# Optimization experiments

Hardware: AMD Instinct MI355X
Metric: run time of the kernel (lower is better)

Reference implementation:

```python
import jax, jax.numpy as jnp
import numpy as np

H = 64  # hidden size


def _gru_cell(x, h, Wih, Whh, bih, bhh):
    """PyTorch-convention GRU cell. x:[B,in], h:[B,H]. Gate order: r, z, n."""
    gi = x @ Wih.T + bih              # [B, 3H]
    gh = h @ Whh.T + bhh              # [B, 3H]
    ir, iz, in_ = jnp.split(gi, 3, axis=-1)
    hr, hz, hn = jnp.split(gh, 3, axis=-1)
    r = jax.nn.sigmoid(ir + hr)
    z = jax.nn.sigmoid(iz + hz)
    n = jnp.tanh(in_ + r * hn)
    return (1.0 - z) * n + z * h


def setup_inputs() -> dict:
    key = jax.random.key(0)
    B, T, NIN = 4096, 256, 6
    ks = jax.random.split(key, 24)

    def w(k, shape, fan):
        return (jax.random.normal(k, shape, jnp.float32) / np.sqrt(fan).astype(np.float32))

    inp = {"x": jax.random.normal(ks[0], (B, T, NIN), jnp.float32)}
    # encoder layer 0 (input 6) and layer 1 (input 64)
    inp["enc_Wih0"] = w(ks[1], (3 * H, NIN), H)
    inp["enc_Whh0"] = w(ks[2], (3 * H, H), H)
    inp["enc_bih0"] = w(ks[3], (3 * H,), H)
    inp["enc_bhh0"] = w(ks[4], (3 * H,), H)
    inp["enc_Wih1"] = w(ks[5], (3 * H, H), H)
    inp["enc_Whh1"] = w(ks[6], (3 * H, H), H)
    inp["enc_bih1"] = w(ks[7], (3 * H,), H)
    inp["enc_bhh1"] = w(ks[8], (3 * H,), H)
    # decoder layer 0 (input 1) and layer 1 (input 64)
    inp["dec_Wih0"] = w(ks[9], (3 * H, 1), H)
    inp["dec_Whh0"] = w(ks[10], (3 * H, H), H)
    inp["dec_bih0"] = w(ks[11], (3 * H,), H)
    inp["dec_bhh0"] = w(ks[12], (3 * H,), H)
    inp["dec_Wih1"] = w(ks[13], (3 * H, H), H)
    inp["dec_Whh1"] = w(ks[14], (3 * H, H), H)
    inp["dec_bih1"] = w(ks[15], (3 * H,), H)
    inp["dec_bhh1"] = w(ks[16], (3 * H,), H)
    # output head
    inp["out_W"] = w(ks[17], (1, H), H)
    inp["out_b"] = w(ks[18], (1,), H)
    inp["target_len"] = 180
    return inp


def reference(x, enc_Wih0, enc_Whh0, enc_bih0, enc_bhh0,
              enc_Wih1, enc_Whh1, enc_bih1, enc_bhh1,
              dec_Wih0, dec_Whh0, dec_bih0, dec_bhh0,
              dec_Wih1, dec_Whh1, dec_bih1, dec_bhh1,
              out_W, out_b, target_len):
    B = x.shape[0]
    dtype = x.dtype

    # ---- encoder: 2-layer GRU over x, return final hidden per layer ----
    seq = jnp.swapaxes(x, 0, 1)  # [T, B, 6] time-major
    enc_layers = [(enc_Wih0, enc_Whh0, enc_bih0, enc_bhh0),
                  (enc_Wih1, enc_Whh1, enc_bih1, enc_bhh1)]
    h_finals = []
    for (Wih, Whh, bih, bhh) in enc_layers:
        def step(h, xt, Wih=Wih, Whh=Whh, bih=bih, bhh=bhh):
            hn = _gru_cell(xt, h, Wih, Whh, bih, bhh)
            return hn, hn
        h_last, seq = jax.lax.scan(step, jnp.zeros((B, H), dtype), seq)
        h_finals.append(h_last)

    def dec_step(carry, _):
        h0, h1, prev = carry
        h0 = _gru_cell(prev, h0, dec_Wih0, dec_Whh0, dec_bih0, dec_bhh0)
        h1 = _gru_cell(h0, h1, dec_Wih1, dec_Whh1, dec_bih1, dec_bhh1)
        cv = h1 @ out_W.T + out_b  # [B, 1]
        return (h0, h1, cv), cv

    prev0 = jnp.zeros((B, 1), dtype)
    _, outs = jax.lax.scan(dec_step, (h_finals[0], h_finals[1], prev0),
                           None, length=target_len)
    return jnp.swapaxes(outs, 0, 1)  # [B, target_len, 1]
```

## Files before the change

kernel.cpp:

```cpp
#include <hip/hip_runtime.h>
#include <cstdint>

typedef _Float16 half8 __attribute__((ext_vector_type(8)));
typedef __attribute__((ext_vector_type(4))) float floatx4;
typedef unsigned int uint;

#define TSEQ 256
#define TDEC 180
#define NIN  6
#define GROWS 16
#define NBLK (4096 / GROWS)
#define RS0 104
#define RS1 72

__device__ __forceinline__ floatx4 mfma16(half8 a, half8 b, floatx4 c) {
  return __builtin_amdgcn_mfma_f32_16x16x32_f16(a, b, c, 0, 0, 0);
}

__device__ __forceinline__ float sigm(float v) {
  return __builtin_amdgcn_rcpf(1.0f + __builtin_amdgcn_exp2f(-1.4426950408889634f * v));
}
__device__ __forceinline__ float tanh_fast(float v) {
  return 2.0f * __builtin_amdgcn_rcpf(1.0f + __builtin_amdgcn_exp2f(-2.8853900817779268f * v)) - 1.0f;
}

__device__ __forceinline__ half8 ldh8(const _Float16* p) { return *(const half8*)p; }

#define PASS2(F0, F1, r, z, g, W) do {                                  \
  r = mfma16(F0, W[0][0], r); z = mfma16(F0, W[1][0], z); g = mfma16(F0, W[2][0], g); \
  r = mfma16(F1, W[0][1], r); z = mfma16(F1, W[1][1], z); g = mfma16(F1, W[2][1], g); \
} while (0)

#define PASS1(F0, r, z, g, W) do {                                      \
  r = mfma16(F0, W[0][0], r); z = mfma16(F0, W[1][0], z); g = mfma16(F0, W[2][0], g); \
} while (0)

__device__ __forceinline__ void pollge1(const volatile uint* p, uint need4) {
  for (;;) {
    if (*p >= need4) break;
    __builtin_amdgcn_s_sleep(1);
  }
  asm volatile("" ::: "memory");
}

__global__ void __launch_bounds__(512, 2)
gru_persist(const float* __restrict__ x,
            const float* __restrict__ eWih0, const float* __restrict__ eWhh0,
            const float* __restrict__ ebih0, const float* __restrict__ ebhh0,
            const float* __restrict__ eWih1, const float* __restrict__ eWhh1,
            const float* __restrict__ ebih1, const float* __restrict__ ebhh1,
            const float* __restrict__ dWih0, const float* __restrict__ dWhh0,
            const float* __restrict__ dbih0, const float* __restrict__ dbhh0,
            const float* __restrict__ dWih1, const float* __restrict__ dWhh1,
            const float* __restrict__ dbih1, const float* __restrict__ dbhh1,
            const float* __restrict__ outW, const float* __restrict__ outB,
            float* __restrict__ out)
{
  __shared__ __align__(16) _Float16 s0[2][16][RS0];
  __shared__ __align__(16) _Float16 s1[2][16][RS1];
  __shared__ __align__(16) uint prog[16];

  const int tid  = threadIdx.x;
  const bool isA = tid < 256;
  const int wvL  = (tid >> 6) & 3;
  const int lane = tid & 63;
  const int c    = lane & 15;
  const int q    = lane >> 4;
  const int u    = wvL * 16 + c;
  const long base = (long)blockIdx.x * GROWS;

  const volatile uint* asum = (const volatile uint*)&prog[0];
  const volatile uint* bsum = (const volatile uint*)&prog[8];
  uint* mysum = (uint*)&prog[isA ? 0 : 8];

  for (int i = tid; i < 2 * 16 * RS0; i += 512) ((uint16_t*)s0)[i] = 0;
  for (int i = tid; i < 2 * 16 * RS1; i += 512) ((uint16_t*)s1)[i] = 0;
  if (tid < 16) prog[tid] = 0;
  if (tid < GROWS * NIN) {
    int m = tid / 6, i2 = tid - m * 6;
    s0[0][m][64 + i2] = (_Float16)x[(base + m) * (TSEQ * NIN) + i2];
  }

  half8 W1[3][2];
  half8 W2[3][2];
  float hr[4] = {0, 0, 0, 0};

  auto loadW64 = [&](const float* W, half8 (&D)[3][2]) {
    #pragma unroll
    for (int s = 0; s < 3; s++) {
      const int n = (s * 4 + wvL) * 16 + c;
      #pragma unroll
      for (int kt = 0; kt < 2; kt++) {
        const int k0 = kt * 32 + q * 8;
        #pragma unroll
        for (int j = 0; j < 8; j++) D[s][kt][j] = (_Float16)W[n * 64 + k0 + j];
      }
    }
  };

  float cR, cZ, c3, c4;
  if (isA) {
    loadW64(eWhh0, W1);
    #pragma unroll
    for (int s = 0; s < 3; s++) {
      const int n = (s * 4 + wvL) * 16 + c;
      #pragma unroll
      for (int kt = 0; kt < 2; kt++)
        #pragma unroll
        for (int j = 0; j < 8; j++) {
          float v = (kt == 0 && q == 0 && j < NIN) ? eWih0[n * NIN + j] : 0.0f;
          W2[s][kt][j] = (_Float16)v;
        }
    }
    cR = ebih0[u] + ebhh0[u];
    cZ = ebih0[64 + u] + ebhh0[64 + u];
    c3 = ebhh0[128 + u];
    c4 = ebih0[128 + u];
  } else {
    loadW64(eWih1, W1); loadW64(eWhh1, W2);
    cR = ebih1[u] + ebhh1[u];
    cZ = ebih1[64 + u] + ebhh1[64 + u];
    c3 = ebih1[128 + u];
    c4 = ebhh1[128 + u];
  }
  __syncthreads();

  if (isA) {
    const bool doX = (wvL == 0) && (lane < 48);
    const float *px0 = nullptr, *px1 = nullptr;
    int xo0 = 0, xo1 = 0; float xn0 = 0.f, xn1 = 0.f;
    if (doX) {
      int s0_ = lane, s1_ = lane + 48;
      int m0 = s0_ / 6, i0 = s0_ - m0 * 6, m1 = s1_ / 6, i1 = s1_ - m1 * 6;
      px0 = x + (base + m0) * (TSEQ * NIN) + i0;
      px1 = x + (base + m1) * (TSEQ * NIN) + i1;
      xo0 = m0 * RS0 + 64 + i0; xo1 = m1 * RS0 + 64 + i1;
      xn0 = px0[NIN]; xn1 = px1[NIN];
    }
    for (int i = 0; i < TSEQ; i += 2) {
      #pragma unroll
      for (int h2 = 0; h2 < 2; h2++) {
        const int i_ = i + h2, p = h2, pn = h2 ^ 1;
        pollge1(asum, 4u * (uint)i_);
        const half8 a0 = ldh8(&s0[p][c][q * 8]);
        const half8 a1 = ldh8(&s0[p][c][32 + q * 8]);
        const half8 xf = ldh8(&s0[p][c][64 + q * 8]);
        floatx4 aR = {cR, cR, cR, cR}, aZ = {cZ, cZ, cZ, cZ};
        floatx4 a3 = {c3, c3, c3, c3}, a4 = {c4, c4, c4, c4};
        PASS2(a0, a1, aR, aZ, a3, W1);
        PASS1(xf, aR, aZ, a4, W2);
        pollge1(bsum, 4u * (uint)(i_ > 0 ? i_ - 1 : 0));
        if (doX && i_ + 1 < TSEQ) {
          ((_Float16*)s0[pn])[xo0] = (_Float16)xn0;
          ((_Float16*)s0[pn])[xo1] = (_Float16)xn1;
          if (i_ + 2 < TSEQ) { xn0 = px0[(i_ + 2) * NIN]; xn1 = px1[(i_ + 2) * NIN]; }
        }
        #pragma unroll
        for (int r4 = 0; r4 < 4; r4++) {
          const float gr = sigm(aR[r4]);
          const float gz = sigm(aZ[r4]);
          const float nn = tanh_fast(a4[r4] + gr * a3[r4]);
          const float hn = nn + gz * (hr[r4] - nn);
          hr[r4] = hn;
          s0[pn][q * 4 + r4][u] = (_Float16)hn;
        }
        asm volatile("s_waitcnt lgkmcnt(0)" ::: "memory");
        if (lane == 0) atomicAdd(mysum, 1u);
      }
    }
    loadW64(dWhh0, W1);
    const float ob = outB[0];
    #pragma unroll
    for (int s = 0; s < 3; s++) {
      const int n = (s * 4 + wvL) * 16 + c;
      const float wd = dWih0[n];
      #pragma unroll
      for (int kt = 0; kt < 2; kt++) {
        const int k0 = kt * 32 + q * 8;
        #pragma unroll
        for (int j = 0; j < 8; j++) W2[s][kt][j] = (_Float16)(wd * outW[k0 + j]);
      }
    }
    const float bR0 = dbih0[u] + dbhh0[u];
    const float bZ0 = dbih0[64 + u] + dbhh0[64 + u];
    const float b30 = dbhh0[128 + u];
    const float b40 = dbih0[128 + u];
    cR = bR0 + dWih0[u] * ob;
    cZ = bZ0 + dWih0[64 + u] * ob;
    c3 = b30;
    c4 = b40 + dWih0[128 + u] * ob;
    for (int i = TSEQ; i < TSEQ + TDEC; i += 2) {
      #pragma unroll
      for (int h2 = 0; h2 < 2; h2++) {
        const int i_ = i + h2, p = h2, pn = h2 ^ 1;
        const bool first = (i_ == TSEQ);
        pollge1(asum, 4u * (uint)i_);
        const half8 a0 = ldh8(&s0[p][c][q * 8]);
        const half8 a1 = ldh8(&s0[p][c][32 + q * 8]);
        const float vR = first ? bR0 : cR, vZ = first ? bZ0 : cZ, v4 = first ? b40 : c4;
        floatx4 aR = {vR, vR, vR, vR}, aZ = {vZ, vZ, vZ, vZ};
        floatx4 a3 = {c3, c3, c3, c3}, a4 = {v4, v4, v4, v4};
        PASS2(a0, a1, aR, aZ, a3, W1);
        pollge1(bsum, 4u * (uint)(first ? i_ - 1 : i_));
        if (!first) {
          const half8 b0 = ldh8(&s1[p][c][q * 8]);
          const half8 b1 = ldh8(&s1[p][c][32 + q * 8]);
          PASS2(b0, b1, aR, aZ, a4, W2);
        }
        #pragma unroll
        for (int r4 = 0; r4 < 4; r4++) {
          const float gr = sigm(aR[r4]);
          const float gz = sigm(aZ[r4]);
          const float nn = tanh_fast(a4[r4] + gr * a3[r4]);
          const float hn = nn + gz * (hr[r4] - nn);
          hr[r4] = hn;
          s0[pn][q * 4 + r4][u] = (_Float16)hn;
        }
        asm volatile("s_waitcnt lgkmcnt(0)" ::: "memory");
        if (lane == 0) atomicAdd(mysum, 1u);
      }
    }
  } else {
    const float ob = outB[0];
    float wk[2][8];
    #pragma unroll
    for (int kt = 0; kt < 2; kt++)
      #pragma unroll
      for (int j = 0; j < 8; j++) wk[kt][j] = outW[kt * 32 + q * 8 + j];

    for (int i = 0; i < TSEQ; i += 2) {
      #pragma unroll
      for (int h2 = 0; h2 < 2; h2++) {
        const int i_ = i + h2, p = h2, pn = h2 ^ 1;
        pollge1(bsum, 4u * (uint)i_);
        const half8 f0 = ldh8(&s1[p][c][q * 8]);
        const half8 f1 = ldh8(&s1[p][c][32 + q * 8]);
        floatx4 aR = {cR, cR, cR, cR}, aZ = {cZ, cZ, cZ, cZ};
        floatx4 a3 = {c3, c3, c3, c3}, a4 = {c4, c4, c4, c4};
        PASS2(f0, f1, aR, aZ, a4, W2);
        pollge1(asum, 4u * (uint)(i_ + 1));
        const half8 g0 = ldh8(&s0[pn][c][q * 8]);
        const half8 g1 = ldh8(&s0[pn][c][32 + q * 8]);
        PASS2(g0, g1, aR, aZ, a3, W1);
        #pragma unroll
        for (int r4 = 0; r4 < 4; r4++) {
          const float gr = sigm(aR[r4]);
          const float gz = sigm(aZ[r4]);
          const float nn = tanh_fast(a3[r4] + gr * a4[r4]);
          const float hn = nn + gz * (hr[r4] - nn);
          hr[r4] = hn;
          s1[pn][q * 4 + r4][u] = (_Float16)hn;
        }
        asm volatile("s_waitcnt lgkmcnt(0)" ::: "memory");
        if (lane == 0) atomicAdd(mysum, 1u);
      }
    }
    loadW64(dWih1, W1); loadW64(dWhh1, W2);
    cR = dbih1[u] + dbhh1[u];
    cZ = dbih1[64 + u] + dbhh1[64 + u];
    c3 = dbih1[128 + u]; c4 = dbhh1[128 + u];
    for (int i = TSEQ; i < TSEQ + TDEC; i += 2) {
      #pragma unroll
      for (int h2 = 0; h2 < 2; h2++) {
        const int i_ = i + h2, p = h2, pn = h2 ^ 1;
        pollge1(bsum, 4u * (uint)i_);
        const half8 f0 = ldh8(&s1[p][c][q * 8]);
        const half8 f1 = ldh8(&s1[p][c][32 + q * 8]);
        floatx4 aR = {cR, cR, cR, cR}, aZ = {cZ, cZ, cZ, cZ};
        floatx4 a3 = {c3, c3, c3, c3}, a4 = {c4, c4, c4, c4};
        PASS2(f0, f1, aR, aZ, a4, W2);
        if (wvL == 0 && i_ > TSEQ) {
          float cv = 0.0f;
          #pragma unroll
          for (int j = 0; j < 8; j++) {
            cv = fmaf((float)f0[j], wk[0][j], cv);
            cv = fmaf((float)f1[j], wk[1][j], cv);
          }
          cv += __shfl_xor(cv, 16);
          cv += __shfl_xor(cv, 32);
          if (lane < 16) out[(base + lane) * TDEC + (i_ - TSEQ - 1)] = cv + ob;
        }
        pollge1(asum, 4u * (uint)(i_ + 1));
        const half8 g0 = ldh8(&s0[pn][c][q * 8]);
        const half8 g1 = ldh8(&s0[pn][c][32 + q * 8]);
        PASS2(g0, g1, aR, aZ, a3, W1);
        #pragma unroll
        for (int r4 = 0; r4 < 4; r4++) {
          const float gr = sigm(aR[r4]);
          const float gz = sigm(aZ[r4]);
          const float nn = tanh_fast(a3[r4] + gr * a4[r4]);
          const float hn = nn + gz * (hr[r4] - nn);
          hr[r4] = hn;
          s1[pn][q * 4 + r4][u] = (_Float16)hn;
        }
        asm volatile("s_waitcnt lgkmcnt(0)" ::: "memory");
        if (lane == 0) atomicAdd(mysum, 1u);
      }
    }
    if (wvL == 0) {
      pollge1(bsum, 4u * (uint)(TSEQ + TDEC));
      const half8 f0 = ldh8(&s1[0][c][q * 8]);
      const half8 f1 = ldh8(&s1[0][c][32 + q * 8]);
      float cv = 0.0f;
      #pragma unroll
      for (int j = 0; j < 8; j++) {
        cv = fmaf((float)f0[j], wk[0][j], cv);
        cv = fmaf((float)f1[j], wk[1][j], cv);
      }
      cv += __shfl_xor(cv, 16);
      cv += __shfl_xor(cv, 32);
      if (lane < 16) out[(base + lane) * TDEC + (TDEC - 1)] = cv + ob;
    }
  }
}

extern "C" void kernel_launch(void* const* d_in, const int* in_sizes, int n_in,
                              void* d_out, int out_size, void* d_ws, size_t ws_size,
                              hipStream_t stream) {
  (void)in_sizes; (void)n_in; (void)d_ws; (void)ws_size; (void)out_size;
  const float* x     = (const float*)d_in[0];
  const float* eWih0 = (const float*)d_in[1];
  const float* eWhh0 = (const float*)d_in[2];
  const float* ebih0 = (const float*)d_in[3];
  const float* ebhh0 = (const float*)d_in[4];
  const float* eWih1 = (const float*)d_in[5];
  const float* eWhh1 = (const float*)d_in[6];
  const float* ebih1 = (const float*)d_in[7];
  const float* ebhh1 = (const float*)d_in[8];
  const float* dWih0 = (const float*)d_in[9];
  const float* dWhh0 = (const float*)d_in[10];
  const float* dbih0 = (const float*)d_in[11];
  const float* dbhh0 = (const float*)d_in[12];
  const float* dWih1 = (const float*)d_in[13];
  const float* dWhh1 = (const float*)d_in[14];
  const float* dbih1 = (const float*)d_in[15];
  const float* dbhh1 = (const float*)d_in[16];
  const float* outW  = (const float*)d_in[17];
  const float* outB  = (const float*)d_in[18];
  hipLaunchKernelGGL(gru_persist, dim3(NBLK), dim3(512), 0, stream,
                     x, eWih0, eWhh0, ebih0, ebhh0, eWih1, eWhh1, ebih1, ebhh1,
                     dWih0, dWhh0, dbih0, dbhh0, dWih1, dWhh1, dbih1, dbhh1,
                     outW, outB, (float*)d_out);
}
```

Baseline: 411.0 us.

## Fold log2e scaling into weights, preload bias accumulators, peel first decoder steps

Pre-scales the gate weights and biases by log2(e) (twice that for the candidate gate) so sigmoid and tanh become exp2 calls with no per-element multiply. Bias vectors are kept as loop-invariant accumulator registers and fed as the MFMA C operand, which removes the per-step splat initialisation. The first two decoder steps of layer 0 are peeled so the steady-state loop has no 'first' branches. It also drops the explicit lgkmcnt(0) wait before the progress atomic and keeps only a compiler barrier, which risks a race if the LDS writes are not complete when the counter is published.

```diff
diff --git a/kernel.cpp b/kernel.cpp
--- a/kernel.cpp
+++ b/kernel.cpp
@@ -12,27 +12,33 @@
 #define NBLK (4096 / GROWS)
 #define RS0 104
 #define RS1 72
+#define L2E 1.4426950408889634f
 
 __device__ __forceinline__ floatx4 mfma16(half8 a, half8 b, floatx4 c) {
   return __builtin_amdgcn_mfma_f32_16x16x32_f16(a, b, c, 0, 0, 0);
 }
 
-__device__ __forceinline__ float sigm(float v) {
-  return __builtin_amdgcn_rcpf(1.0f + __builtin_amdgcn_exp2f(-1.4426950408889634f * v));
-}
-__device__ __forceinline__ float tanh_fast(float v) {
-  return 2.0f * __builtin_amdgcn_rcpf(1.0f + __builtin_amdgcn_exp2f(-2.8853900817779268f * v)) - 1.0f;
+__device__ __forceinline__ float sigm2(float v) {
+  return __builtin_amdgcn_rcpf(1.0f + __builtin_amdgcn_exp2f(-v));
+}
+__device__ __forceinline__ float tanh2(float v) {
+  return fmaf(2.0f, __builtin_amdgcn_rcpf(1.0f + __builtin_amdgcn_exp2f(-v)), -1.0f);
 }
 
 __device__ __forceinline__ half8 ldh8(const _Float16* p) { return *(const half8*)p; }
 
-#define PASS2(F0, F1, r, z, g, W) do {                                  \
-  r = mfma16(F0, W[0][0], r); z = mfma16(F0, W[1][0], z); g = mfma16(F0, W[2][0], g); \
-  r = mfma16(F1, W[0][1], r); z = mfma16(F1, W[1][1], z); g = mfma16(F1, W[2][1], g); \
+#define PASS2_I3(F0, F1, r, z, g, W, QR, QZ, QG) do {                   \
+  r = mfma16(F0, W[0][0], QR); z = mfma16(F0, W[1][0], QZ); g = mfma16(F0, W[2][0], QG); \
+  r = mfma16(F1, W[0][1], r);  z = mfma16(F1, W[1][1], z);  g = mfma16(F1, W[2][1], g);  \
 } while (0)
 
-#define PASS1(F0, r, z, g, W) do {                                      \
-  r = mfma16(F0, W[0][0], r); z = mfma16(F0, W[1][0], z); g = mfma16(F0, W[2][0], g); \
+#define PASS2_A2I1(F0, F1, r, z, g, W, QG) do {                         \
+  r = mfma16(F0, W[0][0], r); z = mfma16(F0, W[1][0], z); g = mfma16(F0, W[2][0], QG); \
+  r = mfma16(F1, W[0][1], r); z = mfma16(F1, W[1][1], z); g = mfma16(F1, W[2][1], g);  \
+} while (0)
+
+#define PASS1_A2I1(F0, r, z, g, W, QG) do {                             \
+  r = mfma16(F0, W[0][0], r); z = mfma16(F0, W[1][0], z); g = mfma16(F0, W[2][0], QG); \
 } while (0)
 
 __device__ __forceinline__ void pollge1(const volatile uint* p, uint need4) {
@@ -42,6 +48,8 @@
   }
   asm volatile("" ::: "memory");
 }
+
+#define PUBLISH() do { asm volatile("" ::: "memory"); if (lane == 0) atomicAdd(mysum, 1u); } while (0)
 
 __global__ void __launch_bounds__(512, 2)
 gru_persist(const float* __restrict__ x,
@@ -84,6 +92,7 @@
   half8 W1[3][2];
   half8 W2[3][2];
   float hr[4] = {0, 0, 0, 0};
+  const float SC[3] = {L2E, L2E, 2.0f * L2E};
 
   auto loadW64 = [&](const float* W, half8 (&D)[3][2]) {
     #pragma unroll
@@ -93,7 +102,7 @@
       for (int kt = 0; kt < 2; kt++) {
         const int k0 = kt * 32 + q * 8;
         #pragma unroll
-        for (int j = 0; j < 8; j++) D[s][kt][j] = (_Float16)W[n * 64 + k0 + j];
+        for (int j = 0; j < 8; j++) D[s][kt][j] = (_Float16)(SC[s] * W[n * 64 + k0 + j]);
       }
     }
   };
@@ -108,24 +117,26 @@
       for (int kt = 0; kt < 2; kt++)
         #pragma unroll
         for (int j = 0; j < 8; j++) {
-          float v = (kt == 0 && q == 0 && j < NIN) ? eWih0[n * NIN + j] : 0.0f;
+          float v = (kt == 0 && q == 0 && j < NIN) ? SC[s] * eWih0[n * NIN + j] : 0.0f;
           W2[s][kt][j] = (_Float16)v;
         }
     }
-    cR = ebih0[u] + ebhh0[u];
-    cZ = ebih0[64 + u] + ebhh0[64 + u];
-    c3 = ebhh0[128 + u];
-    c4 = ebih0[128 + u];
+    cR = L2E * (ebih0[u] + ebhh0[u]);
+    cZ = L2E * (ebih0[64 + u] + ebhh0[64 + u]);
+    c3 = 2.0f * L2E * ebhh0[128 + u];
+    c4 = 2.0f * L2E * ebih0[128 + u];
   } else {
     loadW64(eWih1, W1); loadW64(eWhh1, W2);
-    cR = ebih1[u] + ebhh1[u];
-    cZ = ebih1[64 + u] + ebhh1[64 + u];
-    c3 = ebih1[128 + u];
-    c4 = ebhh1[128 + u];
+    cR = L2E * (ebih1[u] + ebhh1[u]);
+    cZ = L2E * (ebih1[64 + u] + ebhh1[64 + u]);
+    c3 = 2.0f * L2E * ebih1[128 + u];
+    c4 = 2.0f * L2E * ebhh1[128 + u];
   }
   __syncthreads();
 
   if (isA) {
+    floatx4 QR = {cR, cR, cR, cR}, QZ = {cZ, cZ, cZ, cZ};
+    floatx4 Q3 = {c3, c3, c3, c3}, Q4 = {c4, c4, c4, c4};
     const bool doX = (wvL == 0) && (lane < 48);
     const float *px0 = nullptr, *px1 = nullptr;
     int xo0 = 0, xo1 = 0; float xn0 = 0.f, xn1 = 0.f;
@@ -145,10 +156,9 @@
         const half8 a0 = ldh8(&s0[p][c][q * 8]);
         const half8 a1 = ldh8(&s0[p][c][32 + q * 8]);
         const half8 xf = ldh8(&s0[p][c][64 + q * 8]);
-        floatx4 aR = {cR, cR, cR, cR}, aZ = {cZ, cZ, cZ, cZ};
-        floatx4 a3 = {c3, c3, c3, c3}, a4 = {c4, c4, c4, c4};
-        PASS2(a0, a1, aR, aZ, a3, W1);
-        PASS1(xf, aR, aZ, a4, W2);
+        floatx4 aR, aZ, a3, a4;
+        PASS2_I3(a0, a1, aR, aZ, a3, W1, QR, QZ, Q3);
+        PASS1_A2I1(xf, aR, aZ, a4, W2, Q4);
         pollge1(bsum, 4u * (uint)(i_ > 0 ? i_ - 1 : 0));
         if (doX && i_ + 1 < TSEQ) {
           ((_Float16*)s0[pn])[xo0] = (_Float16)xn0;
@@ -157,15 +167,14 @@
         }
         #pragma unroll
         for (int r4 = 0; r4 < 4; r4++) {
-          const float gr = sigm(aR[r4]);
-          const float gz = sigm(aZ[r4]);
-          const float nn = tanh_fast(a4[r4] + gr * a3[r4]);
+          const float gr = sigm2(aR[r4]);
+          const float gz = sigm2(aZ[r4]);
+          const float nn = tanh2(a4[r4] + gr * a3[r4]);
           const float hn = nn + gz * (hr[r4] - nn);
           hr[r4] = hn;
           s0[pn][q * 4 + r4][u] = (_Float16)hn;
         }
-        asm volatile("s_waitcnt lgkmcnt(0)" ::: "memory");
-        if (lane == 0) atomicAdd(mysum, 1u);
+        PUBLISH();
       }
     }
     loadW64(dWhh0, W1);
@@ -173,7 +182,7 @@
     #pragma unroll
     for (int s = 0; s < 3; s++) {
       const int n = (s * 4 + wvL) * 16 + c;
-      const float wd = dWih0[n];
+      const float wd = SC[s] * dWih0[n];
       #pragma unroll
       for (int kt = 0; kt < 2; kt++) {
         const int k0 = kt * 32 + q * 8;
@@ -181,46 +190,86 @@
         for (int j = 0; j < 8; j++) W2[s][kt][j] = (_Float16)(wd * outW[k0 + j]);
       }
     }
-    const float bR0 = dbih0[u] + dbhh0[u];
-    const float bZ0 = dbih0[64 + u] + dbhh0[64 + u];
-    const float b30 = dbhh0[128 + u];
-    const float b40 = dbih0[128 + u];
-    cR = bR0 + dWih0[u] * ob;
-    cZ = bZ0 + dWih0[64 + u] * ob;
+    const float bR0 = L2E * (dbih0[u] + dbhh0[u]);
+    const float bZ0 = L2E * (dbih0[64 + u] + dbhh0[64 + u]);
+    const float b30 = 2.0f * L2E * dbhh0[128 + u];
+    const float b40 = 2.0f * L2E * dbih0[128 + u];
+    cR = bR0 + L2E * (dWih0[u] * ob);
+    cZ = bZ0 + L2E * (dWih0[64 + u] * ob);
     c3 = b30;
-    c4 = b40 + dWih0[128 + u] * ob;
-    for (int i = TSEQ; i < TSEQ + TDEC; i += 2) {
+    c4 = b40 + 2.0f * L2E * (dWih0[128 + u] * ob);
+    QR = (floatx4){cR, cR, cR, cR}; QZ = (floatx4){cZ, cZ, cZ, cZ};
+    Q3 = (floatx4){c3, c3, c3, c3}; Q4 = (floatx4){c4, c4, c4, c4};
+    {
+      pollge1(asum, 4u * (uint)TSEQ);
+      const half8 a0 = ldh8(&s0[0][c][q * 8]);
+      const half8 a1 = ldh8(&s0[0][c][32 + q * 8]);
+      const floatx4 TR = {bR0, bR0, bR0, bR0}, TZ = {bZ0, bZ0, bZ0, bZ0};
+      const floatx4 T3 = {b30, b30, b30, b30};
+      floatx4 aR, aZ, a3;
+      floatx4 a4 = {b40, b40, b40, b40};
+      PASS2_I3(a0, a1, aR, aZ, a3, W1, TR, TZ, T3);
+      pollge1(bsum, 4u * (uint)(TSEQ - 1));
+      #pragma unroll
+      for (int r4 = 0; r4 < 4; r4++) {
+        const float gr = sigm2(aR[r4]);
+        const float gz = sigm2(aZ[r4]);
+        const float nn = tanh2(a4[r4] + gr * a3[r4]);
+        const float hn = nn + gz * (hr[r4] - nn);
+        hr[r4] = hn;
+        s0[1][q * 4 + r4][u] = (_Float16)hn;
+      }
+      PUBLISH();
+    }
+    {
+      pollge1(asum, 4u * (uint)(TSEQ + 1));
+      const half8 a0 = ldh8(&s0[1][c][q * 8]);
+      const half8 a1 = ldh8(&s0[1][c][32 + q * 8]);
+      floatx4 aR, aZ, a3, a4;
+      PASS2_I3(a0, a1, aR, aZ, a3, W1, QR, QZ, Q3);
+      pollge1(bsum, 4u * (uint)(TSEQ + 1));
+      const half8 b0 = ldh8(&s1[1][c][q * 8]);
+      const half8 b1 = ldh8(&s1[1][c][32 + q * 8]);
+      PASS2_A2I1(b0, b1, aR, aZ, a4, W2, Q4);
+      #pragma unroll
+      for (int r4 = 0; r4 < 4; r4++) {
+        const float gr = sigm2(aR[r4]);
+        const float gz = sigm2(aZ[r4]);
+        const float nn = tanh2(a4[r4] + gr * a3[r4]);
+        const float hn = nn + gz * (hr[r4] - nn);
+        hr[r4] = hn;
+        s0[0][q * 4 + r4][u] = (_Float16)hn;
+      }
+      PUBLISH();
+    }
+    for (int i = TSEQ + 2; i < TSEQ + TDEC; i += 2) {
       #pragma unroll
       for (int h2 = 0; h2 < 2; h2++) {
         const int i_ = i + h2, p = h2, pn = h2 ^ 1;
-        const bool first = (i_ == TSEQ);
         pollge1(asum, 4u * (uint)i_);
         const half8 a0 = ldh8(&s0[p][c][q * 8]);
         const half8 a1 = ldh8(&s0[p][c][32 + q * 8]);
-        const float vR = first ? bR0 : cR, vZ = first ? bZ0 : cZ, v4 = first ? b40 : c4;
-        floatx4 aR = {vR, vR, vR, vR}, aZ = {vZ, vZ, vZ, vZ};
-        floatx4 a3 = {c3, c3, c3, c3}, a4 = {v4, v4, v4, v4};
-        PASS2(a0, a1, aR, aZ, a3, W1);
-        pollge1(bsum, 4u * (uint)(first ? i_ - 1 : i_));
-        if (!first) {
-          const half8 b0 = ldh8(&s1[p][c][q * 8]);
-          const half8 b1 = ldh8(&s1[p][c][32 + q * 8]);
-          PASS2(b0, b1, aR, aZ, a4, W2);
-        }
+        floatx4 aR, aZ, a3, a4;
+        PASS2_I3(a0, a1, aR, aZ, a3, W1, QR, QZ, Q3);
+        pollge1(bsum, 4u * (uint)i_);
+        const half8 b0 = ldh8(&s1[p][c][q * 8]);
+        const half8 b1 = ldh8(&s1[p][c][32 + q * 8]);
+        PASS2_A2I1(b0, b1, aR, aZ, a4, W2, Q4);
         #pragma unroll
         for (int r4 = 0; r4 < 4; r4++) {
-          const float gr = sigm(aR[r4]);
-          const float gz = sigm(aZ[r4]);
-          const float nn = tanh_fast(a4[r4] + gr * a3[r4]);
+          const float gr = sigm2(aR[r4]);
+          const float gz = sigm2(aZ[r4]);
+          const float nn = tanh2(a4[r4] + gr * a3[r4]);
           const float hn = nn + gz * (hr[r4] - nn);
           hr[r4] = hn;
           s0[pn][q * 4 + r4][u] = (_Float16)hn;
         }
-        asm volatile("s_waitcnt lgkmcnt(0)" ::: "memory");
-        if (lane == 0) atomicAdd(mysum, 1u);
+        PUBLISH();
       }
     }
   } else {
+    floatx4 QR = {cR, cR, cR, cR}, QZ = {cZ, cZ, cZ, cZ};
+    floatx4 Q3 = {c3, c3, c3, c3}, Q4 = {c4, c4, c4, c4};
     const float ob = outB[0];
     float wk[2][8];
     #pragma unroll
@@ -235,30 +284,31 @@
         pollge1(bsum, 4u * (uint)i_);
         const half8 f0 = ldh8(&s1[p][c][q * 8]);
         const half8 f1 = ldh8(&s1[p][c][32 + q * 8]);
-        floatx4 aR = {cR, cR, cR, cR}, aZ = {cZ, cZ, cZ, cZ};
-        floatx4 a3 = {c3, c3, c3, c3}, a4 = {c4, c4, c4, c4};
-        PASS2(f0, f1, aR, aZ, a4, W2);
+        floatx4 aR, aZ, a3, a4;
+        PASS2_I3(f0, f1, aR, aZ, a4, W2, QR, QZ, Q4);
         pollge1(asum, 4u * (uint)(i_ + 1));
         const half8 g0 = ldh8(&s0[pn][c][q * 8]);
         const half8 g1 = ldh8(&s0[pn][c][32 + q * 8]);
-        PASS2(g0, g1, aR, aZ, a3, W1);
+        PASS2_A2I1(g0, g1, aR, aZ, a3, W1, Q3);
         #pragma unroll
         for (int r4 = 0; r4 < 4; r4++) {
-          const float gr = sigm(aR[r4]);
-          const float gz = sigm(aZ[r4]);
-          const float nn = tanh_fast(a3[r4] + gr * a4[r4]);
+          const float gr = sigm2(aR[r4]);
+          const float gz = sigm2(aZ[r4]);
+          const float nn = tanh2(a3[r4] + gr * a4[r4]);
           const float hn = nn + gz * (hr[r4] - nn);
           hr[r4] = hn;
           s1[pn][q * 4 + r4][u] = (_Float16)hn;
         }
-        asm volatile("s_waitcnt lgkmcnt(0)" ::: "memory");
-        if (lane == 0) atomicAdd(mysum, 1u);
+        PUBLISH();
       }
     }
     loadW64(dWih1, W1); loadW64(dWhh1, W2);
-    cR = dbih1[u] + dbhh1[u];
-    cZ = dbih1[64 + u] + dbhh1[64 + u];
-    c3 = dbih1[128 + u]; c4 = dbhh1[128 + u];
+    cR = L2E * (dbih1[u] + dbhh1[u]);
+    cZ = L2E * (dbih1[64 + u] + dbhh1[64 + u]);
+    c3 = 2.0f * L2E * dbih1[128 + u];
+    c4 = 2.0f * L2E * dbhh1[128 + u];
+    QR = (floatx4){cR, cR, cR, cR}; QZ = (floatx4){cZ, cZ, cZ, cZ};
+    Q3 = (floatx4){c3, c3, c3, c3}; Q4 = (floatx4){c4, c4, c4, c4};
     for (int i = TSEQ; i < TSEQ + TDEC; i += 2) {
       #pragma unroll
       for (int h2 = 0; h2 < 2; h2++) {
@@ -266,9 +316,8 @@
         pollge1(bsum, 4u * (uint)i_);
         const half8 f0 = ldh8(&s1[p][c][q * 8]);
         const half8 f1 = ldh8(&s1[p][c][32 + q * 8]);
-        floatx4 aR = {cR, cR, cR, cR}, aZ = {cZ, cZ, cZ, cZ};
-        floatx4 a3 = {c3, c3, c3, c3}, a4 = {c4, c4, c4, c4};
-        PASS2(f0, f1, aR, aZ, a4, W2);
+        floatx4 aR, aZ, a3, a4;
+        PASS2_I3(f0, f1, aR, aZ, a4, W2, QR, QZ, Q4);
         if (wvL == 0 && i_ > TSEQ) {
           float cv = 0.0f;
           #pragma unroll
@@ -283,18 +332,17 @@
         pollge1(asum, 4u * (uint)(i_ + 1));
         const half8 g0 = ldh8(&s0[pn][c][q * 8]);
         const half8 g1 = ldh8(&s0[pn][c][32 + q * 8]);
-        PASS2(g0, g1, aR, aZ, a3, W1);
+        PASS2_A2I1(g0, g1, aR, aZ, a3, W1, Q3);
         #pragma unroll
         for (int r4 = 0; r4 < 4; r4++) {
-          const float gr = sigm(aR[r4]);
-          const float gz = sigm(aZ[r4]);
-          const float nn = tanh_fast(a3[r4] + gr * a4[r4]);
+          const float gr = sigm2(aR[r4]);
+          const float gz = sigm2(aZ[r4]);
+          const float nn = tanh2(a3[r4] + gr * a4[r4]);
           const float hn = nn + gz * (hr[r4] - nn);
           hr[r4] = hn;
           s1[pn][q * 4 + r4][u] = (_Float16)hn;
         }
-        asm volatile("s_waitcnt lgkmcnt(0)" ::: "memory");
-        if (lane == 0) atomicAdd(mysum, 1u);
+        PUBLISH();
       }
     }
     if (wvL == 0) {
```

Result: faster. 392.7 us (-4.5%).
